# Performance work log

Hardware: AMD Instinct MI355X
Metric: run time of the kernel (lower is better)

The kernel has to match this reference:

```python
import jax, jax.numpy as jnp
import numpy as np

THRESHOLD = 1.0


def heaviside(x):
    return (x > 0).astype(x.dtype)


def lif_parallel(x, W_ih, b_ih, b_hh, beta):
    """snntorch LeakyParallel: RNN with relu nonlinearity and diagonal
    recurrent weight = beta, followed by threshold spike (no reset).
    x: [T, B, I]; W_ih: [H, I]; beta: [H]. Returns spikes [T, B, H]."""
    beta = jnp.clip(beta, 0.0, 1.0)
    # input projection is time-parallel (one big GEMM)
    z = jnp.einsum('tbi,hi->tbh', x, W_ih) + b_ih + b_hh  # [T, B, H]

    def step(h, z_t):
        h_new = jax.nn.relu(z_t + beta * h)
        return h_new, h_new

    h0 = jnp.zeros(z.shape[1:], z.dtype)
    _, mem = jax.lax.scan(step, h0, z)  # [T, B, H]
    return heaviside(mem - THRESHOLD)


def setup_inputs() -> dict:
    key = jax.random.key(0)
    ks = jax.random.split(key, 9)
    T, B, I, H, O = 200, 256, 784, 1000, 10
    s1 = 1.0 / np.sqrt(I)
    s2 = 1.0 / np.sqrt(H)
    return {
        'x': jax.random.normal(ks[0], (T, B, I), dtype=jnp.float32),
        'W_ih1': jax.random.normal(ks[1], (H, I), dtype=jnp.float32) * s1,
        'b_ih1': jax.random.normal(ks[2], (H,), dtype=jnp.float32) * s1,
        'b_hh1': jax.random.normal(ks[3], (H,), dtype=jnp.float32) * s1,
        'beta1': jnp.full((H,), 0.95, dtype=jnp.float32),
        'W_ih2': jax.random.normal(ks[4], (O, H), dtype=jnp.float32) * s2,
        'b_ih2': jax.random.normal(ks[5], (O,), dtype=jnp.float32) * s2,
        'b_hh2': jax.random.normal(ks[6], (O,), dtype=jnp.float32) * s2,
        'beta2': jnp.full((O,), 0.95, dtype=jnp.float32),
    }


def reference(x, W_ih1, b_ih1, b_hh1, beta1, W_ih2, b_ih2, b_hh2, beta2):
    spk1 = lif_parallel(x, W_ih1, b_ih1, b_hh1, beta1)   # [T, B, 1000]
    spk2 = lif_parallel(spk1, W_ih2, b_ih2, b_hh2, beta2)  # [T, B, 10]
    return spk2
```

## Files before the change

### kernel.cpp

```cpp
#include <hip/hip_runtime.h>
#include <cstdint>
#include <cstddef>

#define T_STEPS 200
#define B_SZ    256
#define I_SZ    784
#define H_SZ    1000
#define O_SZ    10
#define M_ROWS  (T_STEPS * B_SZ)

#define KT        25
#define TILE_WORDS 4096
#define MBLKS     400
#define NBLKS     8

__device__ __forceinline__ int swz32(int g) { return (g & 24) | ((g + (g >> 3)) & 7); }
__device__ __forceinline__ int inv32(int p) { return (p & 24) | ((p - (p >> 3)) & 7); }

typedef const __attribute__((address_space(1))) void gvoid;
typedef __attribute__((address_space(3))) void lvoid;
__device__ __forceinline__ void gload16(const void* g, void* l) {
    __builtin_amdgcn_global_load_lds((gvoid*)g, (lvoid*)l, 16, 0, 0);
}

__global__ __launch_bounds__(256) void pack_kernel(
    const float* __restrict__ src, float* __restrict__ dst, int nrows)
{
    int bid = blockIdx.x;
    int blk = bid / KT, kt = bid - blk * KT;

    __shared__ float T[32 * 132];
    const int tid = threadIdx.x;

    #pragma unroll
    for (int it = 0; it < 4; ++it) {
        int id = tid + it * 256;
        int r  = id >> 3;
        int c4 = id & 7;
        int row = blk * 128 + r;
        int k   = kt * 32 + c4 * 4;
        float4 v = make_float4(0.f, 0.f, 0.f, 0.f);
        if (row < nrows && k < I_SZ)
            v = *(const float4*)(src + (size_t)row * I_SZ + k);
        T[(c4*4 + 0) * 132 + r] = v.x;
        T[(c4*4 + 1) * 132 + r] = v.y;
        T[(c4*4 + 2) * 132 + r] = v.z;
        T[(c4*4 + 3) * 132 + r] = v.w;
    }
    __syncthreads();

    float* out = dst + (size_t)(blk * KT + kt) * TILE_WORDS;
    #pragma unroll
    for (int it = 0; it < 4; ++it) {
        int id = tid + it * 256;
        int k  = id >> 5;
        int pg = id & 31;
        int g  = inv32(pg);
        float4 v = *(const float4*)&T[k * 132 + g * 4];
        *(float4*)(out + k * 128 + pg * 4) = v;
    }
}

__global__ __launch_bounds__(256, 2) void gemm1_v4(
    const float* __restrict__ Xp, const float* __restrict__ Wp,
    const float* __restrict__ b_ih, const float* __restrict__ b_hh,
    float* __restrict__ Z)
{
    __shared__ float Al[2][TILE_WORDS];
    __shared__ float Bl[2][TILE_WORDS];

    const int tid = threadIdx.x;
    const int tr  = tid >> 4;
    const int tc  = tid & 15;

    int bid  = blockIdx.x;
    int wg   = (bid & 7) * 400 + (bid >> 3);
    int mblk = wg >> 3;
    int nblk = wg & 7;
    const int row0 = mblk * 128;
    const int col0 = nblk * 128;

    const int a0 = swz32(2*tr)     * 4;
    const int a1 = swz32(2*tr + 1) * 4;
    const int b0 = swz32(2*tc)     * 4;
    const int b1 = swz32(2*tc + 1) * 4;

    const float* pA = Xp + (size_t)mblk * KT * TILE_WORDS;
    const float* pB = Wp + (size_t)nblk * KT * TILE_WORDS;

    float acc[8][8] = {};

    auto stage = [&](int kt, int b) {
        const float* sA = pA + kt * TILE_WORDS + tid * 4;
        const float* sB = pB + kt * TILE_WORDS + tid * 4;
        gload16(sA,        &Al[b][        tid * 4]);
        gload16(sA + 1024, &Al[b][1024 + tid * 4]);
        gload16(sA + 2048, &Al[b][2048 + tid * 4]);
        gload16(sA + 3072, &Al[b][3072 + tid * 4]);
        gload16(sB,        &Bl[b][        tid * 4]);
        gload16(sB + 1024, &Bl[b][1024 + tid * 4]);
        gload16(sB + 2048, &Bl[b][2048 + tid * 4]);
        gload16(sB + 3072, &Bl[b][3072 + tid * 4]);
    };

    stage(0, 0);
    __syncthreads();

    for (int kt = 0; kt < KT; ++kt) {
        const int cur = kt & 1;
        if (kt + 1 < KT) stage(kt + 1, cur ^ 1);

        const float* A = Al[cur];
        const float* B = Bl[cur];

        #pragma unroll
        for (int k = 0; k < 32; ++k) {
            const float4 A0 = *(const float4*)&A[k*128 + a0];
            const float4 A1 = *(const float4*)&A[k*128 + a1];
            const float4 B0 = *(const float4*)&B[k*128 + b0];
            const float4 B1 = *(const float4*)&B[k*128 + b1];
            #define FMA_ROW(i, av) \
                acc[i][0] = fmaf(av, B0.x, acc[i][0]); \
                acc[i][1] = fmaf(av, B0.y, acc[i][1]); \
                acc[i][2] = fmaf(av, B0.z, acc[i][2]); \
                acc[i][3] = fmaf(av, B0.w, acc[i][3]); \
                acc[i][4] = fmaf(av, B1.x, acc[i][4]); \
                acc[i][5] = fmaf(av, B1.y, acc[i][5]); \
                acc[i][6] = fmaf(av, B1.z, acc[i][6]); \
                acc[i][7] = fmaf(av, B1.w, acc[i][7]);
            FMA_ROW(0, A0.x) FMA_ROW(1, A0.y) FMA_ROW(2, A0.z) FMA_ROW(3, A0.w)
            FMA_ROW(4, A1.x) FMA_ROW(5, A1.y) FMA_ROW(6, A1.z) FMA_ROW(7, A1.w)
            #undef FMA_ROW
        }
        __syncthreads();
    }

    float bias[8];
    #pragma unroll
    for (int j = 0; j < 8; ++j) {
        int cc = col0 + tc * 8 + j;
        bias[j] = (cc < H_SZ) ? (b_ih[cc] + b_hh[cc]) : 0.f;
    }

    const bool full = (col0 + 127 < H_SZ);
    #pragma unroll
    for (int i = 0; i < 8; ++i) {
        int rr = row0 + tr * 8 + i;
        float* zrow = Z + (size_t)rr * H_SZ + col0 + tc * 8;
        if (full) {
            float4 v0 = make_float4(acc[i][0] + bias[0], acc[i][1] + bias[1],
                                    acc[i][2] + bias[2], acc[i][3] + bias[3]);
            float4 v1 = make_float4(acc[i][4] + bias[4], acc[i][5] + bias[5],
                                    acc[i][6] + bias[6], acc[i][7] + bias[7]);
            *(float4*)(zrow + 0) = v0;
            *(float4*)(zrow + 4) = v1;
        } else {
            #pragma unroll
            for (int j = 0; j < 8; ++j) {
                int cc = col0 + tc * 8 + j;
                if (cc < H_SZ) zrow[j] = acc[i][j] + bias[j];
            }
        }
    }
}

__global__ __launch_bounds__(256) void scan1_kernel(
    float* __restrict__ Z, const float* __restrict__ beta)
{
    int idx = blockIdx.x * blockDim.x + threadIdx.x;
    if (idx >= B_SZ * H_SZ) return;
    int h = idx % H_SZ;
    float be = fminf(fmaxf(beta[h], 0.f), 1.f);
    float hm = 0.f;
    const size_t stride = (size_t)B_SZ * H_SZ;
    float* p = Z + idx;
    for (int t = 0; t < T_STEPS; ++t) {
        float v = p[(size_t)t * stride];
        hm = fmaxf(fmaf(be, hm, v), 0.f);
        p[(size_t)t * stride] = (hm > 1.0f) ? 1.0f : 0.0f;
    }
}

__global__ __launch_bounds__(256) void gemm2_kernel(
    const float* __restrict__ S, const float* __restrict__ W2,
    const float* __restrict__ b_ih2, const float* __restrict__ b_hh2,
    float* __restrict__ Z2)
{
    __shared__ float W2s[O_SZ * H_SZ];
    for (int i = threadIdx.x; i < O_SZ * H_SZ; i += blockDim.x)
        W2s[i] = W2[i];
    __syncthreads();

    const int wave  = threadIdx.x >> 6;
    const int lane  = threadIdx.x & 63;
    const int wgid  = blockIdx.x * (blockDim.x >> 6) + wave;
    const int nwave = gridDim.x * (blockDim.x >> 6);

    for (int m = wgid; m < M_ROWS; m += nwave) {
        const float* row = S + (size_t)m * H_SZ;
        float acc[O_SZ];
        #pragma unroll
        for (int o = 0; o < O_SZ; ++o) acc[o] = 0.f;

        for (int h = lane; h < H_SZ; h += 64) {
            float s = row[h];
            #pragma unroll
            for (int o = 0; o < O_SZ; ++o)
                acc[o] = fmaf(s, W2s[o * H_SZ + h], acc[o]);
        }
        #pragma unroll
        for (int o = 0; o < O_SZ; ++o) {
            float v = acc[o];
            #pragma unroll
            for (int off = 32; off > 0; off >>= 1)
                v += __shfl_down(v, off, 64);
            if (lane == 0)
                Z2[(size_t)m * O_SZ + o] = v + b_ih2[o] + b_hh2[o];
        }
    }
}

#define CH 20
__global__ __launch_bounds__(256) void scan2_kernel(
    float* __restrict__ Z2io, const float* __restrict__ beta2)
{
    int idx = blockIdx.x * blockDim.x + threadIdx.x;
    if (idx >= B_SZ * O_SZ) return;
    int o = idx % O_SZ;
    float be = fminf(fmaxf(beta2[o], 0.f), 1.f);
    float hm = 0.f;
    const int stride = B_SZ * O_SZ;
    for (int t0 = 0; t0 < T_STEPS; t0 += CH) {
        float v[CH];
        #pragma unroll
        for (int i = 0; i < CH; ++i)
            v[i] = Z2io[(size_t)(t0 + i) * stride + idx];
        #pragma unroll
        for (int i = 0; i < CH; ++i) {
            hm = fmaxf(fmaf(be, hm, v[i]), 0.f);
            Z2io[(size_t)(t0 + i) * stride + idx] = (hm > 1.0f) ? 1.0f : 0.0f;
        }
    }
}

extern "C" void kernel_launch(void* const* d_in, const int* in_sizes, int n_in,
                              void* d_out, int out_size, void* d_ws, size_t ws_size,
                              hipStream_t stream)
{
    const float* x     = (const float*)d_in[0];
    const float* W1    = (const float*)d_in[1];
    const float* bih1  = (const float*)d_in[2];
    const float* bhh1  = (const float*)d_in[3];
    const float* beta1 = (const float*)d_in[4];
    const float* W2    = (const float*)d_in[5];
    const float* bih2  = (const float*)d_in[6];
    const float* bhh2  = (const float*)d_in[7];
    const float* beta2 = (const float*)d_in[8];
    float* out = (float*)d_out;

    char* base = (char*)d_ws;
    float* z1 = (float*)base;
    float* Xp = (float*)(base + (size_t)M_ROWS * H_SZ * 4);
    float* Wp = Xp + (size_t)MBLKS * KT * TILE_WORDS;

    pack_kernel<<<MBLKS * KT, 256, 0, stream>>>(x,  Xp, M_ROWS);
    pack_kernel<<<NBLKS * KT, 256, 0, stream>>>(W1, Wp, H_SZ);

    gemm1_v4<<<MBLKS * NBLKS, 256, 0, stream>>>(Xp, Wp, bih1, bhh1, z1);

    scan1_kernel<<<(B_SZ * H_SZ) / 256, 256, 0, stream>>>(z1, beta1);
    gemm2_kernel<<<2048, 256, 0, stream>>>(z1, W2, bih2, bhh2, out);
    scan2_kernel<<<(B_SZ * O_SZ + 255) / 256, 256, 0, stream>>>(out, beta2);
}
```

Measured before the change: 1.267 ms.

## Enlarge GEMM1 block tile to 256x128 with 16x8 per-thread accumulators

Each block of the first GEMM now computes a 256x128 output tile from two packed A tiles and one B tile, so each thread holds 16x8 accumulators instead of 8x8. This halves the block count and the number of W tile reloads, and raises FMA work per LDS read of B. In exchange it drops the double-buffered LDS prefetch: each k-step loads into one buffer, syncs, then computes, so global load latency is exposed. Register pressure also rises, which may limit occupancy under the two-blocks-per-SM launch bound.

```diff
diff --git a/kernel.cpp b/kernel.cpp
--- a/kernel.cpp
+++ b/kernel.cpp
@@ -13,6 +13,7 @@
 #define TILE_WORDS 4096
 #define MBLKS     400
 #define NBLKS     8
+#define MBLK2S    200
 
 __device__ __forceinline__ int swz32(int g) { return (g & 24) | ((g + (g >> 3)) & 7); }
 __device__ __forceinline__ int inv32(int p) { return (p & 24) | ((p - (p >> 3)) & 7); }
@@ -61,64 +62,64 @@
     }
 }
 
-__global__ __launch_bounds__(256, 2) void gemm1_v4(
+__global__ __launch_bounds__(256, 2) void gemm1_v5(
     const float* __restrict__ Xp, const float* __restrict__ Wp,
     const float* __restrict__ b_ih, const float* __restrict__ b_hh,
     float* __restrict__ Z)
 {
-    __shared__ float Al[2][TILE_WORDS];
-    __shared__ float Bl[2][TILE_WORDS];
-
-    const int tid = threadIdx.x;
-    const int tr  = tid >> 4;
-    const int tc  = tid & 15;
-
-    int bid  = blockIdx.x;
-    int wg   = (bid & 7) * 400 + (bid >> 3);
-    int mblk = wg >> 3;
-    int nblk = wg & 7;
-    const int row0 = mblk * 128;
+    __shared__ float Alds[32 * 256];
+    __shared__ float Blds[32 * 128];
+
+    const int tid  = threadIdx.x;
+    const int w    = tid >> 6;
+    const int lane = tid & 63;
+    const int tr   = tid >> 4;
+    const int tc   = tid & 15;
+
+    int bid   = blockIdx.x;
+    int wg    = (bid & 7) * 200 + (bid >> 3);
+    int mblk2 = wg >> 3;
+    int nblk  = wg & 7;
+    const int row0 = mblk2 * 256;
     const int col0 = nblk * 128;
 
-    const int a0 = swz32(2*tr)     * 4;
-    const int a1 = swz32(2*tr + 1) * 4;
-    const int b0 = swz32(2*tc)     * 4;
-    const int b1 = swz32(2*tc + 1) * 4;
-
-    const float* pA = Xp + (size_t)mblk * KT * TILE_WORDS;
-    const float* pB = Wp + (size_t)nblk * KT * TILE_WORDS;
-
-    float acc[8][8] = {};
-
-    auto stage = [&](int kt, int b) {
-        const float* sA = pA + kt * TILE_WORDS + tid * 4;
-        const float* sB = pB + kt * TILE_WORDS + tid * 4;
-        gload16(sA,        &Al[b][        tid * 4]);
-        gload16(sA + 1024, &Al[b][1024 + tid * 4]);
-        gload16(sA + 2048, &Al[b][2048 + tid * 4]);
-        gload16(sA + 3072, &Al[b][3072 + tid * 4]);
-        gload16(sB,        &Bl[b][        tid * 4]);
-        gload16(sB + 1024, &Bl[b][1024 + tid * 4]);
-        gload16(sB + 2048, &Bl[b][2048 + tid * 4]);
-        gload16(sB + 3072, &Bl[b][3072 + tid * 4]);
-    };
-
-    stage(0, 0);
-    __syncthreads();
+    const int ahalf = (tr >> 3) * 128;
+    int aoff0 = ahalf + swz32((tr & 7) * 4 + 0) * 4;
+    int aoff1 = ahalf + swz32((tr & 7) * 4 + 1) * 4;
+    int aoff2 = ahalf + swz32((tr & 7) * 4 + 2) * 4;
+    int aoff3 = ahalf + swz32((tr & 7) * 4 + 3) * 4;
+    const int b0 = swz32(2 * tc)     * 4;
+    const int b1 = swz32(2 * tc + 1) * 4;
+
+    const float* pA0 = Xp + (size_t)(mblk2 * 2    ) * KT * TILE_WORDS;
+    const float* pA1 = Xp + (size_t)(mblk2 * 2 + 1) * KT * TILE_WORDS;
+    const float* pB  = Wp + (size_t)nblk * KT * TILE_WORDS;
+
+    const float* aSrc = (lane < 32 ? pA0 : pA1) + w * 128 + (lane & 31) * 4;
+
+    float acc[16][8] = {};
 
     for (int kt = 0; kt < KT; ++kt) {
-        const int cur = kt & 1;
-        if (kt + 1 < KT) stage(kt + 1, cur ^ 1);
-
-        const float* A = Al[cur];
-        const float* B = Bl[cur];
-
-        #pragma unroll
+        const float* aS = aSrc + kt * TILE_WORDS;
+        const float* bS = pB + kt * TILE_WORDS + tid * 4;
+        #pragma unroll
+        for (int i = 0; i < 8; ++i)
+            gload16(aS + i * 512, &Alds[i * 1024 + tid * 4]);
+        #pragma unroll
+        for (int i = 0; i < 4; ++i)
+            gload16(bS + i * 1024, &Blds[i * 1024 + tid * 4]);
+        __syncthreads();
+
+        #pragma unroll 4
         for (int k = 0; k < 32; ++k) {
-            const float4 A0 = *(const float4*)&A[k*128 + a0];
-            const float4 A1 = *(const float4*)&A[k*128 + a1];
-            const float4 B0 = *(const float4*)&B[k*128 + b0];
-            const float4 B1 = *(const float4*)&B[k*128 + b1];
+            const float* Ak = &Alds[k * 256];
+            const float* Bk = &Blds[k * 128];
+            const float4 A0 = *(const float4*)&Ak[aoff0];
+            const float4 A1 = *(const float4*)&Ak[aoff1];
+            const float4 A2 = *(const float4*)&Ak[aoff2];
+            const float4 A3 = *(const float4*)&Ak[aoff3];
+            const float4 B0 = *(const float4*)&Bk[b0];
+            const float4 B1 = *(const float4*)&Bk[b1];
             #define FMA_ROW(i, av) \
                 acc[i][0] = fmaf(av, B0.x, acc[i][0]); \
                 acc[i][1] = fmaf(av, B0.y, acc[i][1]); \
@@ -128,8 +129,10 @@
                 acc[i][5] = fmaf(av, B1.y, acc[i][5]); \
                 acc[i][6] = fmaf(av, B1.z, acc[i][6]); \
                 acc[i][7] = fmaf(av, B1.w, acc[i][7]);
-            FMA_ROW(0, A0.x) FMA_ROW(1, A0.y) FMA_ROW(2, A0.z) FMA_ROW(3, A0.w)
-            FMA_ROW(4, A1.x) FMA_ROW(5, A1.y) FMA_ROW(6, A1.z) FMA_ROW(7, A1.w)
+            FMA_ROW( 0, A0.x) FMA_ROW( 1, A0.y) FMA_ROW( 2, A0.z) FMA_ROW( 3, A0.w)
+            FMA_ROW( 4, A1.x) FMA_ROW( 5, A1.y) FMA_ROW( 6, A1.z) FMA_ROW( 7, A1.w)
+            FMA_ROW( 8, A2.x) FMA_ROW( 9, A2.y) FMA_ROW(10, A2.z) FMA_ROW(11, A2.w)
+            FMA_ROW(12, A3.x) FMA_ROW(13, A3.y) FMA_ROW(14, A3.z) FMA_ROW(15, A3.w)
             #undef FMA_ROW
         }
         __syncthreads();
@@ -144,21 +147,21 @@
 
     const bool full = (col0 + 127 < H_SZ);
     #pragma unroll
-    for (int i = 0; i < 8; ++i) {
-        int rr = row0 + tr * 8 + i;
+    for (int s = 0; s < 16; ++s) {
+        int rr = row0 + tr * 16 + s;
         float* zrow = Z + (size_t)rr * H_SZ + col0 + tc * 8;
         if (full) {
-            float4 v0 = make_float4(acc[i][0] + bias[0], acc[i][1] + bias[1],
-                                    acc[i][2] + bias[2], acc[i][3] + bias[3]);
-            float4 v1 = make_float4(acc[i][4] + bias[4], acc[i][5] + bias[5],
-                                    acc[i][6] + bias[6], acc[i][7] + bias[7]);
+            float4 v0 = make_float4(acc[s][0] + bias[0], acc[s][1] + bias[1],
+                                    acc[s][2] + bias[2], acc[s][3] + bias[3]);
+            float4 v1 = make_float4(acc[s][4] + bias[4], acc[s][5] + bias[5],
+                                    acc[s][6] + bias[6], acc[s][7] + bias[7]);
             *(float4*)(zrow + 0) = v0;
             *(float4*)(zrow + 4) = v1;
         } else {
             #pragma unroll
             for (int j = 0; j < 8; ++j) {
                 int cc = col0 + tc * 8 + j;
-                if (cc < H_SZ) zrow[j] = acc[i][j] + bias[j];
+                if (cc < H_SZ) zrow[j] = acc[s][j] + bias[j];
             }
         }
     }
@@ -266,7 +269,7 @@
     pack_kernel<<<MBLKS * KT, 256, 0, stream>>>(x,  Xp, M_ROWS);
     pack_kernel<<<NBLKS * KT, 256, 0, stream>>>(W1, Wp, H_SZ);
 
-    gemm1_v4<<<MBLKS * NBLKS, 256, 0, stream>>>(Xp, Wp, bih1, bhh1, z1);
+    gemm1_v5<<<MBLK2S * NBLKS, 256, 0, stream>>>(Xp, Wp, bih1, bhh1, z1);
 
     scan1_kernel<<<(B_SZ * H_SZ) / 256, 256, 0, stream>>>(z1, beta1);
     gemm2_kernel<<<2048, 256, 0, stream>>>(z1, W2, bih2, bhh2, out);
```

After: 1.236 ms. 1.03x faster.
